# Optimization experiments

Measured on AMD Instinct MI355X. Metric: run time of the kernel, lower is better.

Reference implementation:

```python
import jax, jax.numpy as jnp
import numpy as np

ROPE_BASE = 10000.0
NUM_HEADS = 16
NUM_KV_HEADS = 4


def _rms_norm(x, eps):
    # F.rms_norm with no weight: x / sqrt(mean(x^2) + eps)
    return x * jax.lax.rsqrt(jnp.mean(x * x, axis=-1, keepdims=True) + eps)


def _apply_rope(x, cos, sin):
    h = x.shape[-1] // 2
    x1, x2 = x[..., :h], x[..., h:]
    return jnp.concatenate([x1 * cos + x2 * sin, -x1 * sin + x2 * cos], axis=-1)


def setup_inputs() -> dict:
    key = jax.random.key(0)
    ks = jax.random.split(key, 5)
    B, T, D = 2, 2048, 1024
    H, Hkv = NUM_HEADS, NUM_KV_HEADS
    hd = D // H
    kv_dim = Hkv * hd
    s_in = 1.0 / np.sqrt(D)
    return {
        "x": jax.random.normal(ks[0], (B, T, D), dtype=jnp.float32),
        "Wq": jax.random.normal(ks[1], (D, D), dtype=jnp.float32) * s_in,
        "Wk": jax.random.normal(ks[2], (kv_dim, D), dtype=jnp.float32) * s_in,
        "Wv": jax.random.normal(ks[3], (kv_dim, D), dtype=jnp.float32) * s_in,
        "Wproj": jax.random.normal(ks[4], (D, D), dtype=jnp.float32) * s_in,
        "q_gain": jnp.full((H,), 1.0, dtype=jnp.float32),
    }


def reference(x, Wq, Wk, Wv, Wproj, q_gain):
    B, T, D = x.shape
    H, Hkv = NUM_HEADS, NUM_KV_HEADS
    hd = D // H
    rep = H // Hkv
    eps = jnp.finfo(x.dtype).eps

    # QKV projections (F.linear: x @ W.T)
    q = jnp.einsum('btd,od->bto', x, Wq).reshape(B, T, H, hd).transpose(0, 2, 1, 3)
    k = jnp.einsum('btd,od->bto', x, Wk).reshape(B, T, Hkv, hd).transpose(0, 2, 1, 3)
    v = jnp.einsum('btd,od->bto', x, Wv).reshape(B, T, Hkv, hd).transpose(0, 2, 1, 3)

    q = _rms_norm(q, eps)
    k = _rms_norm(k, eps)

    # RoPE tables: [1, 1, T, hd/2]
    inv_freq = 1.0 / (ROPE_BASE ** (jnp.arange(0, hd, 2, dtype=jnp.float32) / hd))
    f = jnp.arange(T, dtype=jnp.float32)[:, None] * inv_freq[None, :]
    cos = jnp.cos(f)[None, None].astype(q.dtype)
    sin = jnp.sin(f)[None, None].astype(q.dtype)
    q = _apply_rope(q, cos, sin)
    k = _apply_rope(k, cos, sin)

    q = q * q_gain.astype(q.dtype)[None, :, None, None]

    # GQA without materializing repeated K/V: group q heads [Hkv, rep]
    qg = q.reshape(B, Hkv, rep, T, hd)
    scale = hd ** -0.5
    scores = jnp.einsum('bgrqd,bgkd->bgrqk', qg, k) * scale
    causal = jnp.tril(jnp.ones((T, T), dtype=bool))
    scores = jnp.where(causal, scores, -jnp.inf)
    att = jax.nn.softmax(scores.astype(jnp.float32), axis=-1).astype(q.dtype)
    y = jnp.einsum('bgrqk,bgkd->bgrqd', att, v)  # [B,Hkv,rep,T,hd]
    y = y.reshape(B, H, T, hd).transpose(0, 2, 1, 3).reshape(B, T, D)
    return jnp.einsum('btd,od->bto', y, Wproj)
```

## Files before the change

kernel.cpp:

```cpp
#include <hip/hip_runtime.h>
#include <cstdint>
#include <cstddef>

typedef __attribute__((ext_vector_type(8))) short short8;
typedef __attribute__((ext_vector_type(4))) float floatx4;
typedef __attribute__((ext_vector_type(4))) short short4v;
typedef unsigned short u16;
typedef unsigned int u32;

#define B_   2
#define T_   2048
#define D_   1024
#define H_   16
#define HKV_ 4
#define HD_  64
#define KV_  256
#define M_   4096
#define QS_  1536

#define NX   4194304
#define NWQ  1048576
#define NWK  262144
#define NWV  262144
#define NWP  1048576
#define NCAST (NX + NWQ + NWK + NWV + NWP)
#define CAST_BLOCKS (NCAST / 1024)
#define TAB_BLOCKS  256

__device__ __forceinline__ float b2f(u16 u) {
    union { u32 i; float f; } v; v.i = ((u32)u) << 16; return v.f;
}
__device__ __forceinline__ u16 f2b(float f) {
    union { float f; u32 i; } v; v.f = f;
    u32 r = v.i + 0x7FFF + ((v.i >> 16) & 1);
    return (u16)(r >> 16);
}
__device__ __forceinline__ u32 pack_hi(float a, float b) {
    union { float f; u32 u; } ua, ub; ua.f = a; ub.f = b;
    return (ua.u >> 16) | (ub.u & 0xFFFF0000u);
}

__device__ __forceinline__ void async16(const u16* g, u16* l) {
    __builtin_amdgcn_global_load_lds(
        (const __attribute__((address_space(1))) u32*)g,
        (__attribute__((address_space(3))) u32*)l, 16, 0, 0);
}

__global__ __launch_bounds__(256) void prep(const float* __restrict__ x,
                                            const float* __restrict__ wq,
                                            const float* __restrict__ wk,
                                            const float* __restrict__ wv,
                                            const float* __restrict__ wp,
                                            u16* __restrict__ dst,
                                            float2* __restrict__ tab) {
    int blk = blockIdx.x;
    if (blk < CAST_BLOCKS) {
        int i = blk * 1024 + threadIdx.x * 4;
        const float* src; int off;
        if      (i < NX)                  { src = x;  off = i; }
        else if (i < NX+NWQ)              { src = wq; off = i - NX; }
        else if (i < NX+NWQ+NWK)          { src = wk; off = i - (NX+NWQ); }
        else if (i < NX+NWQ+NWK+NWV)      { src = wv; off = i - (NX+NWQ+NWK); }
        else                              { src = wp; off = i - (NX+NWQ+NWK+NWV); }
        float4 v = *(const float4*)(src + off);
        short4v o;
        o.x = (short)f2b(v.x); o.y = (short)f2b(v.y);
        o.z = (short)f2b(v.z); o.w = (short)f2b(v.w);
        *(short4v*)(dst + i) = o;
    } else {
        int idx = (blk - CAST_BLOCKS) * 256 + threadIdx.x;
        int t = idx >> 5, i = idx & 31;
        float freq = exp2f(-(float)i * (13.287712379549449f / 32.0f));
        float ang = (float)t * freq;
        tab[idx] = make_float2(cosf(ang), sinf(ang));
    }
}

__global__ __launch_bounds__(256, 3) void gemm_qkv(const u16* __restrict__ A,
                                                   const u16* __restrict__ W,
                                                   u16* __restrict__ C,
                                                   u16* __restrict__ Vt,
                                                   const float* __restrict__ gain,
                                                   const float2* __restrict__ tab) {
    const int K = D_;
    __shared__ u16 As[2][128 * 32];
    __shared__ u16 Bs[2][64 * 32];
    const int t = threadIdx.x;
    const int wave = t >> 6, lane = t & 63;
    const int quad = lane >> 4, l16 = lane & 15;
    const int wm = wave * 32;
    const int m0 = blockIdx.y * 128, n0 = blockIdx.x * 64;

    floatx4 acc[2][4];
#pragma unroll
    for (int i = 0; i < 2; i++)
#pragma unroll
        for (int j = 0; j < 4; j++) acc[i][j] = (floatx4){0.f, 0.f, 0.f, 0.f};

    const int sr = t >> 2, sc = (t & 3) * 8;
    const u16* ga = A + (size_t)(m0 + sr) * K + sc;
    const u16* gb = W + (size_t)(n0 + sr) * K + sc;

    async16(ga, As[0] + t * 8);
    async16(ga + (size_t)64 * K, As[0] + t * 8 + 64 * 32);
    async16(gb, Bs[0] + t * 8);

    int cur = 0;
    for (int kt = 0; kt < K; kt += 32) {
        __syncthreads();
        if (kt + 32 < K) {
            const u16* ga2 = ga + kt + 32;
            const u16* gb2 = gb + kt + 32;
            async16(ga2, As[cur ^ 1] + t * 8);
            async16(ga2 + (size_t)64 * K, As[cur ^ 1] + t * 8 + 64 * 32);
            async16(gb2, Bs[cur ^ 1] + t * 8);
        }
        short8 af[2], bf[4];
#pragma unroll
        for (int mt = 0; mt < 2; mt++)
            af[mt] = *(const short8*)(As[cur] + (wm + mt * 16 + l16) * 32 + quad * 8);
#pragma unroll
        for (int nt = 0; nt < 4; nt++)
            bf[nt] = *(const short8*)(Bs[cur] + (nt * 16 + l16) * 32 + quad * 8);
#pragma unroll
        for (int mt = 0; mt < 2; mt++)
#pragma unroll
            for (int nt = 0; nt < 4; nt++)
                acc[mt][nt] = __builtin_amdgcn_mfma_f32_16x16x32_bf16(
                    af[mt], bf[nt], acc[mt][nt], 0, 0, 0);
        cur ^= 1;
    }

    const int col0 = n0;
    if (col0 < 1280) {
        float gs = (col0 < 1024)
                 ? gain[col0 >> 6] * (0.125f * 1.4426950408889634f)
                 : 1.0f;
#pragma unroll
        for (int mt = 0; mt < 2; mt++)
#pragma unroll
            for (int r = 0; r < 4; r++) {
                int row = m0 + wm + mt * 16 + quad * 4 + r;
                int tt = row & (T_ - 1);
                float v0 = acc[mt][0][r], v1 = acc[mt][1][r];
                float v2 = acc[mt][2][r], v3 = acc[mt][3][r];
                float ss = v0 * v0 + v1 * v1 + v2 * v2 + v3 * v3;
                ss += __shfl_xor(ss, 1); ss += __shfl_xor(ss, 2);
                ss += __shfl_xor(ss, 4); ss += __shfl_xor(ss, 8);
                float inv = rsqrtf(ss * (1.0f / 64.0f) + 1.1920929e-7f);
                v0 *= inv; v1 *= inv; v2 *= inv; v3 *= inv;
                float2 cs0 = tab[tt * 32 + l16];
                float2 cs1 = tab[tt * 32 + 16 + l16];
                float o0 = (v0 * cs0.x + v2 * cs0.y) * gs;
                float o1 = (v1 * cs1.x + v3 * cs1.y) * gs;
                float o2 = (v2 * cs0.x - v0 * cs0.y) * gs;
                float o3 = (v3 * cs1.x - v1 * cs1.y) * gs;
                u16* cp = C + (size_t)row * QS_ + col0 + l16;
                cp[0]  = f2b(o0);
                cp[16] = f2b(o1);
                cp[32] = f2b(o2);
                cp[48] = f2b(o3);
            }
    } else {
        const int g = (col0 - 1280) >> 6;
#pragma unroll
        for (int mt = 0; mt < 2; mt++)
#pragma unroll
            for (int r = 0; r < 4; r++) {
                int row = m0 + wm + mt * 16 + quad * 4 + r;
                int tt = row & (T_ - 1);
                int bb = row >> 11;
#pragma unroll
                for (int nt = 0; nt < 4; nt++)
                    Vt[(size_t)((bb * 4 + g) * 64 + nt * 16 + l16) * T_ + tt] =
                        f2b(acc[mt][nt][r]);
            }
    }
}

__global__ __launch_bounds__(256, 4) void gemm_proj(const u16* __restrict__ A,
                                                    const u16* __restrict__ W,
                                                    float* __restrict__ C) {
    const int K = D_;
    __shared__ u16 As[2][128 * 32];
    __shared__ u16 Bs[2][64 * 32];
    const int t = threadIdx.x;
    const int wave = t >> 6, lane = t & 63;
    const int quad = lane >> 4, l16 = lane & 15;
    const int wm = wave * 32;
    const int m0 = blockIdx.y * 128, n0 = blockIdx.x * 64;
    const int kbase = blockIdx.z * 512;

    floatx4 acc[2][4];
#pragma unroll
    for (int i = 0; i < 2; i++)
#pragma unroll
        for (int j = 0; j < 4; j++) acc[i][j] = (floatx4){0.f, 0.f, 0.f, 0.f};

    const int sr = t >> 2, sc = (t & 3) * 8;
    const u16* ga = A + (size_t)(m0 + sr) * K + kbase + sc;
    const u16* gb = W + (size_t)(n0 + sr) * K + kbase + sc;

    async16(ga, As[0] + t * 8);
    async16(ga + (size_t)64 * K, As[0] + t * 8 + 64 * 32);
    async16(gb, Bs[0] + t * 8);

    int cur = 0;
    for (int kt = 0; kt < 512; kt += 32) {
        __syncthreads();
        if (kt + 32 < 512) {
            const u16* ga2 = ga + kt + 32;
            const u16* gb2 = gb + kt + 32;
            async16(ga2, As[cur ^ 1] + t * 8);
            async16(ga2 + (size_t)64 * K, As[cur ^ 1] + t * 8 + 64 * 32);
            async16(gb2, Bs[cur ^ 1] + t * 8);
        }
        short8 af[2], bf[4];
#pragma unroll
        for (int mt = 0; mt < 2; mt++)
            af[mt] = *(const short8*)(As[cur] + (wm + mt * 16 + l16) * 32 + quad * 8);
#pragma unroll
        for (int nt = 0; nt < 4; nt++)
            bf[nt] = *(const short8*)(Bs[cur] + (nt * 16 + l16) * 32 + quad * 8);
#pragma unroll
        for (int mt = 0; mt < 2; mt++)
#pragma unroll
            for (int nt = 0; nt < 4; nt++)
                acc[mt][nt] = __builtin_amdgcn_mfma_f32_16x16x32_bf16(
                    af[mt], bf[nt], acc[mt][nt], 0, 0, 0);
        cur ^= 1;
    }

#pragma unroll
    for (int mt = 0; mt < 2; mt++)
#pragma unroll
        for (int nt = 0; nt < 4; nt++)
#pragma unroll
            for (int r = 0; r < 4; r++) {
                int row = m0 + wm + mt * 16 + quad * 4 + r;
                int col = n0 + nt * 16 + l16;
                atomicAdd(&C[(size_t)row * D_ + col], acc[mt][nt][r]);
            }
}

__global__ __launch_bounds__(256, 4) void flash(const u16* __restrict__ QKV,
                                                const u16* __restrict__ Vtr,
                                                u16* __restrict__ Y,
                                                float* __restrict__ Opart,
                                                float* __restrict__ Lpart) {
    const int u  = blockIdx.x;
    const int h  = blockIdx.y;
    const int b  = blockIdx.z;
    const int g  = h >> 2;
    const int w    = threadIdx.x >> 6;
    const int lane = threadIdx.x & 63;
    const int quad = lane >> 4, l16 = lane & 15;

    __shared__ u16 Kt[64 * 64];
    __shared__ u16 Vs[64 * 64];
    __shared__ __align__(16) u16 P[4][16][72];

    const int xp = u & 15;
    const int nseg = (u < 16) ? 2 : 1;
    const int buf  = (u < 16) ? 0 : 1;
    int m0s[2], k0s[2], k1s[2];
    if (u < 16) {
        m0s[0] = xp * 64;        k0s[0] = 0;  k1s[0] = xp + 1;
        m0s[1] = (31 - xp) * 64; k0s[1] = 16; k1s[1] = 32 - xp;
    } else {
        m0s[0] = (31 - xp) * 64; k0s[0] = 0;  k1s[0] = 16;
        m0s[1] = 0; k0s[1] = 0; k1s[1] = 0;
    }

    const int srow = w * 16 + (lane >> 3);
    const int sseg = (lane & 7) ^ ((lane >> 3) & 7);
    const u16* kgb = QKV + (size_t)(b * T_ + srow) * QS_ + D_ + g * 64 + sseg * 8;
    const u16* vgb = Vtr + (size_t)((b * 4 + g) * 64 + srow) * T_ + sseg * 8;
    u16* klds = Kt + w * 1024 + lane * 8;
    u16* vlds = Vs + w * 1024 + lane * 8;
    const int sw0 = (quad ^ (l16 & 7)) * 8;
    const int sw1 = ((4 + quad) ^ (l16 & 7)) * 8;

    auto stage = [&](int tile) {
        const u16* kg = kgb + (size_t)tile * 64 * QS_;
        const u16* vg = vgb + (size_t)tile * 64;
        async16(kg, klds);
        async16(kg + (size_t)8 * QS_, klds + 512);
        async16(vg, vlds);
        async16(vg + (size_t)8 * T_, vlds + 512);
    };

    short8 ones;
#pragma unroll
    for (int i = 0; i < 8; i++) ones[i] = (short)0x3F80;

    stage(k0s[0]);

    for (int seg = 0; seg < nseg; ++seg) {
        const int mseg = m0s[seg], k0 = k0s[seg], k1 = k1s[seg];
        const int jt = mseg >> 6;
        const int m = mseg + w * 16;

        const u16* qp = QKV + (size_t)(b * T_ + m + l16) * QS_ + h * HD_ + quad * 8;
        short8 aq0 = *(const short8*)(qp);
        short8 aq1 = *(const short8*)(qp + 32);

        floatx4 acc[4];
#pragma unroll
        for (int i = 0; i < 4; i++) acc[i] = (floatx4){0.f, 0.f, 0.f, 0.f};
        floatx4 lAcc = (floatx4){0.f, 0.f, 0.f, 0.f};

        for (int tk = k0; tk < k1; ++tk) {
            __syncthreads();

            floatx4 S[4];
#pragma unroll
            for (int nt = 0; nt < 4; nt++) {
                const u16* kr = Kt + (nt * 16 + l16) * 64;
                short8 kf0 = *(const short8*)(kr + sw0);
                short8 kf1 = *(const short8*)(kr + sw1);
                S[nt] = (floatx4){0.f, 0.f, 0.f, 0.f};
                S[nt] = __builtin_amdgcn_mfma_f32_16x16x32_bf16(kf0, aq0, S[nt], 0, 0, 0);
                S[nt] = __builtin_amdgcn_mfma_f32_16x16x32_bf16(kf1, aq1, S[nt], 0, 0, 0);
            }
            short8 vf[4][2];
#pragma unroll
            for (int dd = 0; dd < 4; dd++) {
                const u16* vr = Vs + (dd * 16 + l16) * 64;
                vf[dd][0] = *(const short8*)(vr + sw0);
                vf[dd][1] = *(const short8*)(vr + sw1);
            }
            __syncthreads();

            int nxt = (tk + 1 < k1) ? tk + 1 : ((seg + 1 < nseg) ? k0s[seg + 1] : -1);
            if (nxt >= 0) stage(nxt);

            const bool msk = (tk == jt);
            const int qq = m + l16;
#pragma unroll
            for (int nt = 0; nt < 4; nt++) {
                float p[4];
#pragma unroll
                for (int r = 0; r < 4; r++) {
                    float e = __builtin_amdgcn_exp2f(S[nt][r]);
                    if (msk) {
                        int key = tk * 64 + nt * 16 + quad * 4 + r;
                        e = (key <= qq) ? e : 0.f;
                    }
                    p[r] = e;
                }
                uint2 pw; pw.x = pack_hi(p[0], p[1]); pw.y = pack_hi(p[2], p[3]);
                *(uint2*)&P[w][l16][nt * 16 + quad * 4] = pw;
            }
            short8 pf0 = *(const short8*)&P[w][l16][quad * 8];
            short8 pf1 = *(const short8*)&P[w][l16][quad * 8 + 32];
#pragma unroll
            for (int dd = 0; dd < 4; dd++) {
                acc[dd] = __builtin_amdgcn_mfma_f32_16x16x32_bf16(pf0, vf[dd][0], acc[dd], 0, 0, 0);
                acc[dd] = __builtin_amdgcn_mfma_f32_16x16x32_bf16(pf1, vf[dd][1], acc[dd], 0, 0, 0);
            }
            lAcc = __builtin_amdgcn_mfma_f32_16x16x32_bf16(pf0, ones, lAcc, 0, 0, 0);
            lAcc = __builtin_amdgcn_mfma_f32_16x16x32_bf16(pf1, ones, lAcc, 0, 0, 0);
        }

        if (u < 16 && seg == 0) {
#pragma unroll
            for (int r = 0; r < 4; r++) {
                float inv = 1.0f / lAcc[r];
                int row = m + quad * 4 + r;
                u16* yp = Y + (size_t)(b * T_ + row) * D_ + h * HD_ + l16;
#pragma unroll
                for (int dd = 0; dd < 4; dd++)
                    yp[dd * 16] = f2b(acc[dd][r] * inv);
            }
        } else {
#pragma unroll
            for (int r = 0; r < 4; r++) {
                int rp = m + quad * 4 + r - 1024;
                float* op = Opart + ((size_t)((buf * 2 + b) * 1024 + rp)) * 1024
                          + h * HD_ + l16;
#pragma unroll
                for (int dd = 0; dd < 4; dd++)
                    op[dd * 16] = acc[dd][r];
                if (l16 == 0)
                    Lpart[((buf * 2 + b) * 1024 + rp) * 16 + h] = lAcc[r];
            }
        }
    }
}

__global__ __launch_bounds__(256) void combine(const float* __restrict__ Opart,
                                               const float* __restrict__ Lpart,
                                               u16* __restrict__ Y) {
    int e = (blockIdx.x * 256 + threadIdx.x) * 4;
    int b = e >> 20;
    int rem = e & 1048575;
    int row = rem >> 10, col = rem & 1023;
    int li = (b * 1024 + row) * 16 + (col >> 6);
    float l0 = Lpart[li];
    float l1 = Lpart[li + 2 * 1024 * 16];
    float inv = 1.0f / (l0 + l1);
    size_t oi = ((size_t)(b * 1024 + row)) * 1024 + col;
    float4 o0 = *(const float4*)(Opart + oi);
    float4 o1 = *(const float4*)(Opart + oi + (size_t)2 * 1024 * 1024);
    short4v y;
    y.x = (short)f2b((o0.x + o1.x) * inv); y.y = (short)f2b((o0.y + o1.y) * inv);
    y.z = (short)f2b((o0.z + o1.z) * inv); y.w = (short)f2b((o0.w + o1.w) * inv);
    *(short4v*)(Y + (size_t)(b * T_ + 1024 + row) * D_ + col) = y;
}

extern "C" void kernel_launch(void* const* d_in, const int* in_sizes, int n_in,
                              void* d_out, int out_size, void* d_ws, size_t ws_size,
                              hipStream_t stream) {
    const float* x    = (const float*)d_in[0];
    const float* Wq   = (const float*)d_in[1];
    const float* Wk   = (const float*)d_in[2];
    const float* Wv   = (const float*)d_in[3];
    const float* Wp   = (const float*)d_in[4];
    const float* gain = (const float*)d_in[5];
    float* out = (float*)d_out;

    u16* xb   = (u16*)d_ws;
    u16* Wcat = xb + (size_t)NX;
    u16* Wpb  = Wcat + (size_t)(NWQ + NWK + NWV);
    u16* QKV  = Wpb + (size_t)NWP;
    u16* Vt   = QKV + (size_t)M_ * QS_;
    u16* Y    = Vt + (size_t)M_ * KV_;
    float2* tab = (float2*)(Y + (size_t)M_ * D_);
    float* Opart = (float*)(tab + 65536);
    float* Lpart = Opart + (size_t)4 * 1024 * 1024;

    hipMemsetAsync(out, 0, (size_t)M_ * D_ * 4, stream);

    prep<<<CAST_BLOCKS + TAB_BLOCKS, 256, 0, stream>>>(x, Wq, Wk, Wv, Wp, xb, tab);

    gemm_qkv<<<dim3(QS_ / 64, M_ / 128), 256, 0, stream>>>(xb, Wcat, QKV, Vt,
                                                           gain, tab);

    flash<<<dim3(32, H_, B_), 256, 0, stream>>>(QKV, Vt, Y, Opart, Lpart);

    combine<<<2048, 256, 0, stream>>>(Opart, Lpart, Y);

    gemm_proj<<<dim3(D_ / 64, M_ / 128, 2), 256, 0, stream>>>(Y, Wpb, out);
}
```

Before: 188.4 us.

## Deepen GEMM K-step to 64 and drop split-K atomics in projection

Both GEMMs now stage two 32-wide K slices per pipeline stage, which halves the number of barriers per K loop at the cost of doubled shared memory per block. The projection GEMM stops splitting K across two blocks, so it writes its output with plain stores instead of float atomics, and the output memset is removed. In exchange the projection grid is half as large and each block does twice the K work. Its occupancy hint also drops from 4 to 3 because of the larger LDS footprint.

New measurement: 162.4 us. -13.8%, faster.

```diff
diff --git a/kernel.cpp b/kernel.cpp
--- a/kernel.cpp
+++ b/kernel.cpp
@@ -83,8 +83,8 @@
                                                    const float* __restrict__ gain,
                                                    const float2* __restrict__ tab) {
     const int K = D_;
-    __shared__ u16 As[2][128 * 32];
-    __shared__ u16 Bs[2][64 * 32];
+    __shared__ u16 As[2][2][128 * 32];
+    __shared__ u16 Bs[2][2][64 * 32];
     const int t = threadIdx.x;
     const int wave = t >> 6, lane = t & 63;
     const int quad = lane >> 4, l16 = lane & 15;
@@ -101,33 +101,38 @@
     const u16* ga = A + (size_t)(m0 + sr) * K + sc;
     const u16* gb = W + (size_t)(n0 + sr) * K + sc;
 
-    async16(ga, As[0] + t * 8);
-    async16(ga + (size_t)64 * K, As[0] + t * 8 + 64 * 32);
-    async16(gb, Bs[0] + t * 8);
+    auto stage = [&](int buf, int half, int koff) {
+        async16(ga + koff, As[buf][half] + t * 8);
+        async16(ga + koff + (size_t)64 * K, As[buf][half] + t * 8 + 64 * 32);
+        async16(gb + koff, Bs[buf][half] + t * 8);
+    };
+
+    stage(0, 0, 0);
+    stage(0, 1, 32);
 
     int cur = 0;
-    for (int kt = 0; kt < K; kt += 32) {
+    for (int kt = 0; kt < K; kt += 64) {
         __syncthreads();
-        if (kt + 32 < K) {
-            const u16* ga2 = ga + kt + 32;
-            const u16* gb2 = gb + kt + 32;
-            async16(ga2, As[cur ^ 1] + t * 8);
-            async16(ga2 + (size_t)64 * K, As[cur ^ 1] + t * 8 + 64 * 32);
-            async16(gb2, Bs[cur ^ 1] + t * 8);
-        }
-        short8 af[2], bf[4];
-#pragma unroll
-        for (int mt = 0; mt < 2; mt++)
-            af[mt] = *(const short8*)(As[cur] + (wm + mt * 16 + l16) * 32 + quad * 8);
-#pragma unroll
-        for (int nt = 0; nt < 4; nt++)
-            bf[nt] = *(const short8*)(Bs[cur] + (nt * 16 + l16) * 32 + quad * 8);
-#pragma unroll
-        for (int mt = 0; mt < 2; mt++)
+        if (kt + 64 < K) {
+            stage(cur ^ 1, 0, kt + 64);
+            stage(cur ^ 1, 1, kt + 96);
+        }
+#pragma unroll
+        for (int half = 0; half < 2; half++) {
+            short8 af[2], bf[4];
+#pragma unroll
+            for (int mt = 0; mt < 2; mt++)
+                af[mt] = *(const short8*)(As[cur][half] + (wm + mt * 16 + l16) * 32 + quad * 8);
 #pragma unroll
             for (int nt = 0; nt < 4; nt++)
-                acc[mt][nt] = __builtin_amdgcn_mfma_f32_16x16x32_bf16(
-                    af[mt], bf[nt], acc[mt][nt], 0, 0, 0);
+                bf[nt] = *(const short8*)(Bs[cur][half] + (nt * 16 + l16) * 32 + quad * 8);
+#pragma unroll
+            for (int mt = 0; mt < 2; mt++)
+#pragma unroll
+                for (int nt = 0; nt < 4; nt++)
+                    acc[mt][nt] = __builtin_amdgcn_mfma_f32_16x16x32_bf16(
+                        af[mt], bf[nt], acc[mt][nt], 0, 0, 0);
+        }
         cur ^= 1;
     }
 
@@ -178,18 +183,17 @@
     }
 }
 
-__global__ __launch_bounds__(256, 4) void gemm_proj(const u16* __restrict__ A,
+__global__ __launch_bounds__(256, 3) void gemm_proj(const u16* __restrict__ A,
                                                     const u16* __restrict__ W,
                                                     float* __restrict__ C) {
     const int K = D_;
-    __shared__ u16 As[2][128 * 32];
-    __shared__ u16 Bs[2][64 * 32];
+    __shared__ u16 As[2][2][128 * 32];
+    __shared__ u16 Bs[2][2][64 * 32];
     const int t = threadIdx.x;
     const int wave = t >> 6, lane = t & 63;
     const int quad = lane >> 4, l16 = lane & 15;
     const int wm = wave * 32;
     const int m0 = blockIdx.y * 128, n0 = blockIdx.x * 64;
-    const int kbase = blockIdx.z * 512;
 
     floatx4 acc[2][4];
 #pragma unroll
@@ -198,36 +202,41 @@
         for (int j = 0; j < 4; j++) acc[i][j] = (floatx4){0.f, 0.f, 0.f, 0.f};
 
     const int sr = t >> 2, sc = (t & 3) * 8;
-    const u16* ga = A + (size_t)(m0 + sr) * K + kbase + sc;
-    const u16* gb = W + (size_t)(n0 + sr) * K + kbase + sc;
-
-    async16(ga, As[0] + t * 8);
-    async16(ga + (size_t)64 * K, As[0] + t * 8 + 64 * 32);
-    async16(gb, Bs[0] + t * 8);
+    const u16* ga = A + (size_t)(m0 + sr) * K + sc;
+    const u16* gb = W + (size_t)(n0 + sr) * K + sc;
+
+    auto stage = [&](int buf, int half, int koff) {
+        async16(ga + koff, As[buf][half] + t * 8);
+        async16(ga + koff + (size_t)64 * K, As[buf][half] + t * 8 + 64 * 32);
+        async16(gb + koff, Bs[buf][half] + t * 8);
+    };
+
+    stage(0, 0, 0);
+    stage(0, 1, 32);
 
     int cur = 0;
-    for (int kt = 0; kt < 512; kt += 32) {
+    for (int kt = 0; kt < K; kt += 64) {
         __syncthreads();
-        if (kt + 32 < 512) {
-            const u16* ga2 = ga + kt + 32;
-            const u16* gb2 = gb + kt + 32;
-            async16(ga2, As[cur ^ 1] + t * 8);
-            async16(ga2 + (size_t)64 * K, As[cur ^ 1] + t * 8 + 64 * 32);
-            async16(gb2, Bs[cur ^ 1] + t * 8);
-        }
-        short8 af[2], bf[4];
-#pragma unroll
-        for (int mt = 0; mt < 2; mt++)
-            af[mt] = *(const short8*)(As[cur] + (wm + mt * 16 + l16) * 32 + quad * 8);
-#pragma unroll
-        for (int nt = 0; nt < 4; nt++)
-            bf[nt] = *(const short8*)(Bs[cur] + (nt * 16 + l16) * 32 + quad * 8);
-#pragma unroll
-        for (int mt = 0; mt < 2; mt++)
+        if (kt + 64 < K) {
+            stage(cur ^ 1, 0, kt + 64);
+            stage(cur ^ 1, 1, kt + 96);
+        }
+#pragma unroll
+        for (int half = 0; half < 2; half++) {
+            short8 af[2], bf[4];
+#pragma unroll
+            for (int mt = 0; mt < 2; mt++)
+                af[mt] = *(const short8*)(As[cur][half] + (wm + mt * 16 + l16) * 32 + quad * 8);
 #pragma unroll
             for (int nt = 0; nt < 4; nt++)
-                acc[mt][nt] = __builtin_amdgcn_mfma_f32_16x16x32_bf16(
-                    af[mt], bf[nt], acc[mt][nt], 0, 0, 0);
+                bf[nt] = *(const short8*)(Bs[cur][half] + (nt * 16 + l16) * 32 + quad * 8);
+#pragma unroll
+            for (int mt = 0; mt < 2; mt++)
+#pragma unroll
+                for (int nt = 0; nt < 4; nt++)
+                    acc[mt][nt] = __builtin_amdgcn_mfma_f32_16x16x32_bf16(
+                        af[mt], bf[nt], acc[mt][nt], 0, 0, 0);
+        }
         cur ^= 1;
     }
 
@@ -239,7 +248,7 @@
             for (int r = 0; r < 4; r++) {
                 int row = m0 + wm + mt * 16 + quad * 4 + r;
                 int col = n0 + nt * 16 + l16;
-                atomicAdd(&C[(size_t)row * D_ + col], acc[mt][nt][r]);
+                C[(size_t)row * D_ + col] = acc[mt][nt][r];
             }
 }
 
@@ -430,8 +439,6 @@
     float* Opart = (float*)(tab + 65536);
     float* Lpart = Opart + (size_t)4 * 1024 * 1024;
 
-    hipMemsetAsync(out, 0, (size_t)M_ * D_ * 4, stream);
-
     prep<<<CAST_BLOCKS + TAB_BLOCKS, 256, 0, stream>>>(x, Wq, Wk, Wv, Wp, xb, tab);
 
     gemm_qkv<<<dim3(QS_ / 64, M_ / 128), 256, 0, stream>>>(xb, Wcat, QKV, Vt,
@@ -441,5 +448,5 @@
 
     combine<<<2048, 256, 0, stream>>>(Opart, Lpart, Y);
 
-    gemm_proj<<<dim3(D_ / 64, M_ / 128, 2), 256, 0, stream>>>(Y, Wpb, out);
-}
+    gemm_proj<<<dim3(D_ / 64, M_ / 128), 256, 0, stream>>>(Y, Wpb, out);
+}
```
